# Performance work log

Hardware: AMD Instinct MI355X
Metric: run time of the kernel (lower is better)

## Reference

```python
import jax, jax.numpy as jnp
import numpy as np

B, S, D, E, H, SL = 4, 2048, 2048, 16, 1024, 1
NUM_SLOTS = E * SL
TEMP = 1.0
TOP_K = 2
EPS = 1e-8


def setup_inputs() -> dict:
    key = jax.random.key(0)
    k0, k1, k2, k3 = jax.random.split(key, 4)
    x = jax.random.normal(k0, (B, S, D), dtype=jnp.float32)
    Wd = jax.random.normal(k1, (NUM_SLOTS, D), dtype=jnp.float32) * 0.02
    W1 = jax.random.normal(k2, (E, D, H), dtype=jnp.float32) * 0.02
    b1 = jnp.zeros((E, H), dtype=jnp.float32)
    W2 = jax.random.normal(k3, (E, H, D), dtype=jnp.float32) * 0.02
    b2 = jnp.zeros((E, D), dtype=jnp.float32)
    return {"x": x, "Wd": Wd, "W1": W1, "b1": b1, "W2": W2, "b2": b2}


def reference(x, Wd, W1, b1, W2, b2):
    lead = x.shape[:-1]
    xf = x.reshape(-1, D)                      # [T, D]
    T = xf.shape[0]

    logits = (xf @ Wd.T) / TEMP                # [T, num_slots]
    dispatch = jax.nn.softmax(logits, axis=0)  # softmax over tokens
    combine = jax.nn.softmax(logits, axis=-1)  # softmax over slots

    # Aggregate tokens into slots, run all experts as one batched GEMM chain.
    slot_in = (dispatch.T @ xf).reshape(E, SL, D)                    # [E, SL, D]
    h = jax.nn.gelu(jnp.einsum('esd,edh->esh', slot_in, W1) + b1[:, None, :],
                    approximate=False)
    slot_out = (jnp.einsum('esh,ehd->esd', h, W2) + b2[:, None, :]).reshape(NUM_SLOTS, D)

    out = (combine @ slot_out).reshape(x.shape)

    # Router stats / losses (eval mode: no EMA update of train_scores).
    expert_weights = combine.reshape(T, E, SL).mean(-1)              # [T, E]
    mean_usage = expert_weights.mean(0)                              # [E]
    p = jax.nn.softmax(Wd.mean(0).reshape(E, -1).mean(-1))
    router_loss = E * jnp.sum(mean_usage * p)

    topk_w, topk_idx = jax.lax.top_k(expert_weights, TOP_K)
    topk_w_norm = topk_w / jnp.clip(topk_w.sum(-1, keepdims=True), EPS)

    gate_weights = expert_weights.reshape(*lead, E)
    routing_entropy = -(gate_weights * jnp.log(gate_weights + EPS)).sum(-1).mean()

    return (out,
            router_loss,
            gate_weights,
            topk_idx.reshape(*lead, TOP_K),
            topk_w_norm.reshape(*lead, TOP_K),
            mean_usage,
            routing_entropy,
            dispatch.reshape(*lead, NUM_SLOTS))
```

## Files before the change

kernel.cpp:

```cpp
#include <hip/hip_runtime.h>
#include <math.h>

#define TTOK 8192
#define DIM  2048
#define NH   1024

#define OFF_PART6 0u
#define OFF_NUM   8388608u
#define OFF_COMB  8519680u
#define OFF_CSUM  8650752u
#define OFF_MUSUM 8654848u
#define OFF_ENT   8658944u
#define OFF_SRAW  8659200u
#define OFF_HBUF  8691968u
#define OFF_SLOT  8708352u

#define O_OUT   0u
#define O_LOSS  16777216u
#define O_GATE  16777217u
#define O_TOPI  16908289u
#define O_TOPW  16924673u
#define O_MU    16941057u
#define O_ENTR  16941073u
#define O_DISP  16941074u

__global__ __launch_bounds__(512) void kad(const float* __restrict__ x,
    const float* __restrict__ Wd,
    float* __restrict__ num, float* __restrict__ comb, float* __restrict__ gate_out,
    float* __restrict__ topi_out, float* __restrict__ topw_out,
    float* __restrict__ csum_p, float* __restrict__ musum_p, float* __restrict__ ent_p,
    float* __restrict__ part6){
  const int blk = blockIdx.x;
  const int tid = threadIdx.x;
  const int t0  = blk*32;
  __shared__ float sS[32][17];
  __shared__ __align__(16) float sN[32][16];
  __shared__ float sC[32][16];
  __shared__ float sE[32];

  {
    const int ttp = tid>>5;
    const int kc  = tid&31;
    const float4* xr0 = (const float4*)(x + (size_t)(t0+2*ttp  )*DIM + kc*64);
    const float4* xr1 = (const float4*)(x + (size_t)(t0+2*ttp+1)*DIM + kc*64);
    float a0[16], a1[16];
    #pragma unroll
    for (int e=0;e<16;e++){ a0[e]=0.f; a1[e]=0.f; }
    #pragma unroll
    for (int k4=0;k4<16;k4++){
      float4 x0 = xr0[k4];
      float4 x1 = xr1[k4];
      #pragma unroll
      for (int e=0;e<16;e++){
        float4 w = *(const float4*)(Wd + e*DIM + kc*64 + k4*4);
        a0[e] += x0.x*w.x + x0.y*w.y + x0.z*w.z + x0.w*w.w;
        a1[e] += x1.x*w.x + x1.y*w.y + x1.z*w.z + x1.w*w.w;
      }
    }
    #pragma unroll
    for (int o=1;o<32;o<<=1){
      #pragma unroll
      for (int e=0;e<16;e++){
        a0[e] += __shfl_xor(a0[e],o,64);
        a1[e] += __shfl_xor(a1[e],o,64);
      }
    }
    if (kc==0){
      #pragma unroll
      for (int e=0;e<16;e++){
        sS[2*ttp  ][e] = a0[e];  sN[2*ttp  ][e] = expf(a0[e]);
        sS[2*ttp+1][e] = a1[e];  sN[2*ttp+1][e] = expf(a1[e]);
      }
    }
  }
  __syncthreads();
  if (tid<128) ((float4*)num)[(size_t)blk*128 + tid] = ((const float4*)sN)[tid];
  if (tid<32){
    const int gt = t0 + tid;
    float l[16];
    #pragma unroll
    for (int e=0;e<16;e++) l[e] = sS[tid][e];
    float m = l[0];
    #pragma unroll
    for (int e=1;e<16;e++) m = fmaxf(m,l[e]);
    float c[16]; float sm=0.f;
    #pragma unroll
    for (int e=0;e<16;e++){ c[e]=expf(l[e]-m); sm+=c[e]; }
    float inv = 1.f/sm;
    #pragma unroll
    for (int e=0;e<16;e++) c[e]*=inv;
    float4* co = (float4*)(comb + (size_t)gt*16);
    co[0]=make_float4(c[0],c[1],c[2],c[3]);   co[1]=make_float4(c[4],c[5],c[6],c[7]);
    co[2]=make_float4(c[8],c[9],c[10],c[11]); co[3]=make_float4(c[12],c[13],c[14],c[15]);
    float* go = gate_out + (size_t)gt*16;
    #pragma unroll
    for (int e=0;e<16;e++) go[e]=c[e];
    float v0=-1.f,v1=-1.f; int i0=0,i1=0;
    #pragma unroll
    for (int e=0;e<16;e++){
      float ce=c[e];
      if (ce>v0){ v1=v0;i1=i0; v0=ce;i0=e; }
      else if (ce>v1){ v1=ce;i1=e; }
    }
    float dn = fmaxf(v0+v1,1e-8f);
    topi_out[(size_t)gt*2+0]=(float)i0; topi_out[(size_t)gt*2+1]=(float)i1;
    topw_out[(size_t)gt*2+0]=v0/dn;     topw_out[(size_t)gt*2+1]=v1/dn;
    float ent=0.f;
    #pragma unroll
    for (int e=0;e<16;e++) ent -= c[e]*logf(c[e]+1e-8f);
    sE[tid]=ent;
    #pragma unroll
    for (int e=0;e<16;e++) sC[tid][e]=c[e];
  }
  __syncthreads();
  if (tid<16){
    float ms=0.f, cs=0.f;
    #pragma unroll
    for (int tt=0;tt<32;tt++){ ms += sC[tt][tid]; cs += sN[tt][tid]; }
    musum_p[blk*16+tid]=ms; csum_p[blk*16+tid]=cs;
  }
  if (tid==16){
    float s=0.f;
    #pragma unroll
    for (int k=0;k<32;k++) s += sE[k];
    ent_p[blk]=s;
  }
  __syncthreads();
  {
    float4 acc[16];
    #pragma unroll
    for (int e=0;e<16;e++) acc[e]=make_float4(0,0,0,0);
    #pragma unroll 2
    for (int t=0;t<32;t++){
      const float4 xv = *(const float4*)(x + (size_t)(t0+t)*DIM + tid*4);
      #pragma unroll
      for (int qq=0;qq<4;qq++){
        float4 nq = *((const float4*)&sN[t][qq*4]);
        acc[qq*4+0].x=fmaf(nq.x,xv.x,acc[qq*4+0].x); acc[qq*4+0].y=fmaf(nq.x,xv.y,acc[qq*4+0].y);
        acc[qq*4+0].z=fmaf(nq.x,xv.z,acc[qq*4+0].z); acc[qq*4+0].w=fmaf(nq.x,xv.w,acc[qq*4+0].w);
        acc[qq*4+1].x=fmaf(nq.y,xv.x,acc[qq*4+1].x); acc[qq*4+1].y=fmaf(nq.y,xv.y,acc[qq*4+1].y);
        acc[qq*4+1].z=fmaf(nq.y,xv.z,acc[qq*4+1].z); acc[qq*4+1].w=fmaf(nq.y,xv.w,acc[qq*4+1].w);
        acc[qq*4+2].x=fmaf(nq.z,xv.x,acc[qq*4+2].x); acc[qq*4+2].y=fmaf(nq.z,xv.y,acc[qq*4+2].y);
        acc[qq*4+2].z=fmaf(nq.z,xv.z,acc[qq*4+2].z); acc[qq*4+2].w=fmaf(nq.z,xv.w,acc[qq*4+2].w);
        acc[qq*4+3].x=fmaf(nq.w,xv.x,acc[qq*4+3].x); acc[qq*4+3].y=fmaf(nq.w,xv.y,acc[qq*4+3].y);
        acc[qq*4+3].z=fmaf(nq.w,xv.z,acc[qq*4+3].z); acc[qq*4+3].w=fmaf(nq.w,xv.w,acc[qq*4+3].w);
      }
    }
    #pragma unroll
    for (int e=0;e<16;e++)
      *(float4*)(part6 + ((size_t)blk*16+e)*DIM + tid*4) = acc[e];
  }
}

__global__ __launch_bounds__(256) void ke2(const float* __restrict__ part6,
    const float* __restrict__ csum_p, const float* __restrict__ num,
    const float* __restrict__ musum_p, const float* __restrict__ ent_p,
    const float* __restrict__ Wd,
    float* __restrict__ sraw, float* __restrict__ disp_out,
    float* __restrict__ loss_out, float* __restrict__ mu_out, float* __restrict__ ent_out){
  const int tid = threadIdx.x, blk = blockIdx.x;
  __shared__ float sIv[16][16];
  __shared__ float sInv[16];
  __shared__ float s2[256];
  { int g=tid>>4, e=tid&15;
    float v=0.f;
    #pragma unroll
    for (int k=0;k<16;k++) v += csum_p[(g*16+k)*16 + e];
    sIv[g][e]=v; }
  __syncthreads();
  if (tid<16){
    float v=0.f;
    #pragma unroll
    for (int g=0;g<16;g++) v += sIv[g][tid];
    sInv[tid]=1.f/v;
  }
  __syncthreads();
  { const int ol=tid&31, sl=tid>>5;
    const int o = blk*32 + ol;
    float s=0.f;
    #pragma unroll 8
    for (int k=0;k<32;k++) s += part6[(size_t)(sl*32+k)*32768 + o];
    s2[tid]=s;
  }
  __syncthreads();
  if (tid<32){
    float t=0.f;
    #pragma unroll
    for (int k=0;k<8;k++) t += s2[k*32+tid];
    const int oo = blk*32 + tid;
    sraw[oo] = t * sInv[oo>>11];
  }
  if (blk<512){
    const int t0 = blk*16;
    float v = num[(size_t)t0*16 + tid];
    disp_out[(size_t)t0*16 + tid] = v * sInv[tid&15];
  }
  if (blk==1023){
    __shared__ float sq[16][16];
    __shared__ float smu[16];
    __shared__ float sqv[16];
    __shared__ float sqe[16];
    { int s=tid>>4, ch=tid&15;
      const float* base = Wd + (size_t)s*DIM + ch*128;
      float qv=0.f;
      for (int ii=0;ii<128;ii+=4){ float4 v=*(const float4*)(base+ii); qv+=v.x+v.y+v.z+v.w; }
      sq[s][ch]=qv; }
    if (tid<16){
      float mu=0.f;
      for (int b=0;b<256;b++) mu += musum_p[b*16+tid];
      mu/=8192.f;
      mu_out[tid]=mu; smu[tid]=mu;
    }
    if (tid==32){ float es=0.f; for(int b=0;b<256;b++) es+=ent_p[b]; ent_out[0]=es/8192.f; }
    __syncthreads();
    if (tid<16){ float qv=0.f; for(int s=0;s<16;s++) qv+=sq[s][tid]; sqv[tid]=qv/2048.f; }
    __syncthreads();
    if (tid<16){
      float qm=-INFINITY;
      for (int e=0;e<16;e++) qm=fmaxf(qm,sqv[e]);
      sqe[tid]=expf(sqv[tid]-qm);
    }
    __syncthreads();
    if (tid==0){
      float qs=0.f; for(int e=0;e<16;e++) qs+=sqe[e];
      float loss=0.f; for(int e=0;e<16;e++) loss+=smu[e]*(sqe[e]/qs);
      loss_out[0]=16.f*loss;
    }
  }
}

__global__ __launch_bounds__(256) void kf_h(const float* __restrict__ sraw,
    const float* __restrict__ W1, const float* __restrict__ b1,
    float* __restrict__ hbuf){
  const int e  = blockIdx.x >> 5;
  const int hc = blockIdx.x & 31;
  const int hbase = hc*32;
  const int tid = threadIdx.x;
  __shared__ float sr[2048];
  __shared__ float sacc[256];
  { const float4* s4 = (const float4*)(sraw + (size_t)e*DIM);
    float4 a = s4[tid*2], b = s4[tid*2+1];
    *(float4*)(&sr[tid*8]) = a; *(float4*)(&sr[tid*8+4]) = b; }
  __syncthreads();
  const int hl = tid&31, ds = tid>>5;
  float acc = 0.f;
  const float* wp = W1 + (size_t)e*DIM*NH + hbase + hl;
  #pragma unroll 16
  for (int d2=0; d2<256; d2++){
    const int dd = d2*8 + ds;
    acc = fmaf(sr[dd], wp[(size_t)dd*NH], acc);
  }
  sacc[tid] = acc;
  __syncthreads();
  if (tid < 32){
    float s = 0.f;
    #pragma unroll
    for (int k=0;k<8;k++) s += sacc[k*32 + tid];
    float pre = s + b1[(size_t)e*NH + hbase + tid];
    hbuf[(size_t)e*NH + hbase + tid] = 0.5f*pre*(1.f+erff(pre*0.70710678118654752f));
  }
}

__global__ __launch_bounds__(256) void kg_so(const float* __restrict__ hbuf,
    const float* __restrict__ W2, const float* __restrict__ b2,
    float* __restrict__ slot_out){
  const int e  = blockIdx.x >> 5;
  const int dc = blockIdx.x & 31;
  const int dbase = dc*64;
  const int tid = threadIdx.x;
  __shared__ float hh[1024];
  __shared__ float sacc[256];
  { const float4* h4 = (const float4*)(hbuf + (size_t)e*NH);
    *(float4*)(&hh[tid*4]) = h4[tid]; }
  __syncthreads();
  const int dl = tid&63, hs = tid>>6;
  float acc = 0.f;
  const float* wp = W2 + (size_t)e*NH*DIM + dbase + dl;
  #pragma unroll 16
  for (int h2=0; h2<256; h2++){
    const int hidx = h2*4 + hs;
    acc = fmaf(hh[hidx], wp[(size_t)hidx*DIM], acc);
  }
  sacc[tid] = acc;
  __syncthreads();
  if (tid < 64){
    float s = sacc[tid] + sacc[64+tid] + sacc[128+tid] + sacc[192+tid];
    slot_out[(size_t)e*DIM + dbase + tid] = s + b2[(size_t)e*DIM + dbase + tid];
  }
}

__global__ __launch_bounds__(256) void kh_out(const float* __restrict__ slot_out,
    const float* __restrict__ combine, float* __restrict__ out){
  const int tb = blockIdx.x >> 1;
  const int dc = blockIdx.x & 1;
  const int t0 = tb*16;
  const int d  = dc*1024 + threadIdx.x*4;
  float4 sv[16];
  #pragma unroll
  for (int e=0;e<16;e++) sv[e] = *(const float4*)(slot_out + (size_t)e*DIM + d);
  #pragma unroll 2
  for (int t=0;t<16;t++){
    const float* cr = combine + (size_t)(t0+t)*16;
    float4 a = make_float4(0,0,0,0);
    #pragma unroll
    for (int e=0;e<16;e++){
      float c = cr[e];
      a.x=fmaf(c,sv[e].x,a.x); a.y=fmaf(c,sv[e].y,a.y);
      a.z=fmaf(c,sv[e].z,a.z); a.w=fmaf(c,sv[e].w,a.w);
    }
    *(float4*)(out + (size_t)(t0+t)*DIM + d) = a;
  }
}

extern "C" void kernel_launch(void* const* d_in, const int* in_sizes, int n_in,
                              void* d_out, int out_size, void* d_ws, size_t ws_size,
                              hipStream_t stream) {
  const float* x  = (const float*)d_in[0];
  const float* Wd = (const float*)d_in[1];
  const float* W1 = (const float*)d_in[2];
  const float* b1 = (const float*)d_in[3];
  const float* W2 = (const float*)d_in[4];
  const float* b2 = (const float*)d_in[5];
  float* out = (float*)d_out;
  float* ws  = (float*)d_ws;

  float* part6 = ws + OFF_PART6;
  float* num   = ws + OFF_NUM;
  float* comb  = ws + OFF_COMB;
  float* csump = ws + OFF_CSUM;
  float* musump= ws + OFF_MUSUM;
  float* entp  = ws + OFF_ENT;
  float* sraw  = ws + OFF_SRAW;
  float* hbuf  = ws + OFF_HBUF;
  float* slot  = ws + OFF_SLOT;

  kad<<<256, 512, 0, stream>>>(x, Wd, num, comb, out + O_GATE, out + O_TOPI,
                               out + O_TOPW, csump, musump, entp, part6);
  ke2<<<1024, 256, 0, stream>>>(part6, csump, num, musump, entp, Wd,
                                sraw, out + O_DISP, out + O_LOSS,
                                out + O_MU, out + O_ENTR);
  kf_h<<<512, 256, 0, stream>>>(sraw, W1, b1, hbuf);
  kg_so<<<512, 256, 0, stream>>>(hbuf, W2, b2, slot);
  kh_out<<<1024, 256, 0, stream>>>(slot, comb, out + O_OUT);
}
```

Before: 213.9 us.

## Split fused router kernel into logits, router, and slot-input kernels

Replaces the single 256-block fused kernel with three kernels. The logits kernel runs 1024 blocks that write split-K partial sums to workspace, a router kernel reduces them and computes the softmaxes, top-k and stats, and a slot-input kernel accumulates exp-weighted x across 512 blocks. The goal is more parallelism and occupancy than the fused version with its low block count. The cost is extra kernel launches, a second full read of x, and an 8192x64x16 partial-logit buffer that shares workspace with part6.

New measurement: 204.5 us. -4.4%, faster.

```diff
diff --git a/kernel.cpp b/kernel.cpp
--- a/kernel.cpp
+++ b/kernel.cpp
@@ -5,15 +5,15 @@
 #define DIM  2048
 #define NH   1024
 
-#define OFF_PART6 0u
+#define OFF_ALIAS 0u
 #define OFF_NUM   8388608u
 #define OFF_COMB  8519680u
 #define OFF_CSUM  8650752u
-#define OFF_MUSUM 8654848u
-#define OFF_ENT   8658944u
-#define OFF_SRAW  8659200u
-#define OFF_HBUF  8691968u
-#define OFF_SLOT  8708352u
+#define OFF_MUSUM 8652800u
+#define OFF_ENT   8654848u
+#define OFF_SRAW  8654976u
+#define OFF_HBUF  8687744u
+#define OFF_SLOT  8704128u
 
 #define O_OUT   0u
 #define O_LOSS  16777216u
@@ -24,62 +24,83 @@
 #define O_ENTR  16941073u
 #define O_DISP  16941074u
 
-__global__ __launch_bounds__(512) void kad(const float* __restrict__ x,
-    const float* __restrict__ Wd,
-    float* __restrict__ num, float* __restrict__ comb, float* __restrict__ gate_out,
+__device__ __forceinline__ float wave_sum(float v){
+  #pragma unroll
+  for (int o=1;o<64;o<<=1) v += __shfl_xor(v,o,64);
+  return v;
+}
+
+__global__ __launch_bounds__(256,4) void ka_logits(const float* __restrict__ x,
+                                                   const float* __restrict__ Wd,
+                                                   float* __restrict__ part1){
+  const int tb = blockIdx.x >> 6;
+  const int kc = blockIdx.x & 63;
+  const int t0 = tb*512 + threadIdx.x;
+  const int t1 = t0 + 256;
+  const float4* __restrict__ xr0 = (const float4*)(x + (size_t)t0*DIM + kc*32);
+  const float4* __restrict__ xr1 = (const float4*)(x + (size_t)t1*DIM + kc*32);
+  float a0[16], a1[16];
+  #pragma unroll
+  for (int e=0;e<16;e++){ a0[e]=0.f; a1[e]=0.f; }
+  #pragma unroll
+  for (int k4=0;k4<8;k4++){
+    float4 x0 = xr0[k4];
+    float4 x1 = xr1[k4];
+    #pragma unroll
+    for (int e=0;e<16;e++){
+      float4 w = *(const float4*)(Wd + e*DIM + kc*32 + k4*4);
+      a0[e] += x0.x*w.x + x0.y*w.y + x0.z*w.z + x0.w*w.w;
+      a1[e] += x1.x*w.x + x1.y*w.y + x1.z*w.z + x1.w*w.w;
+    }
+  }
+  float4* p0 = (float4*)(part1 + ((size_t)t0*64 + kc)*16);
+  p0[0]=make_float4(a0[0],a0[1],a0[2],a0[3]);   p0[1]=make_float4(a0[4],a0[5],a0[6],a0[7]);
+  p0[2]=make_float4(a0[8],a0[9],a0[10],a0[11]); p0[3]=make_float4(a0[12],a0[13],a0[14],a0[15]);
+  float4* p1 = (float4*)(part1 + ((size_t)t1*64 + kc)*16);
+  p1[0]=make_float4(a1[0],a1[1],a1[2],a1[3]);   p1[1]=make_float4(a1[4],a1[5],a1[6],a1[7]);
+  p1[2]=make_float4(a1[8],a1[9],a1[10],a1[11]); p1[3]=make_float4(a1[12],a1[13],a1[14],a1[15]);
+}
+
+__global__ __launch_bounds__(256) void kb_router(const float* __restrict__ part1,
+    float* __restrict__ num, float* __restrict__ csum_part,
+    float* __restrict__ combine, float* __restrict__ gate_out,
     float* __restrict__ topi_out, float* __restrict__ topw_out,
-    float* __restrict__ csum_p, float* __restrict__ musum_p, float* __restrict__ ent_p,
-    float* __restrict__ part6){
-  const int blk = blockIdx.x;
+    float* __restrict__ musum_part, float* __restrict__ ent_part){
   const int tid = threadIdx.x;
-  const int t0  = blk*32;
-  __shared__ float sS[32][17];
-  __shared__ __align__(16) float sN[32][16];
-  __shared__ float sC[32][16];
-  __shared__ float sE[32];
-
-  {
-    const int ttp = tid>>5;
-    const int kc  = tid&31;
-    const float4* xr0 = (const float4*)(x + (size_t)(t0+2*ttp  )*DIM + kc*64);
-    const float4* xr1 = (const float4*)(x + (size_t)(t0+2*ttp+1)*DIM + kc*64);
-    float a0[16], a1[16];
-    #pragma unroll
-    for (int e=0;e<16;e++){ a0[e]=0.f; a1[e]=0.f; }
-    #pragma unroll
-    for (int k4=0;k4<16;k4++){
-      float4 x0 = xr0[k4];
-      float4 x1 = xr1[k4];
-      #pragma unroll
-      for (int e=0;e<16;e++){
-        float4 w = *(const float4*)(Wd + e*DIM + kc*64 + k4*4);
-        a0[e] += x0.x*w.x + x0.y*w.y + x0.z*w.z + x0.w*w.w;
-        a1[e] += x1.x*w.x + x1.y*w.y + x1.z*w.z + x1.w*w.w;
-      }
-    }
-    #pragma unroll
-    for (int o=1;o<32;o<<=1){
-      #pragma unroll
-      for (int e=0;e<16;e++){
-        a0[e] += __shfl_xor(a0[e],o,64);
-        a1[e] += __shfl_xor(a1[e],o,64);
-      }
-    }
-    if (kc==0){
-      #pragma unroll
-      for (int e=0;e<16;e++){
-        sS[2*ttp  ][e] = a0[e];  sN[2*ttp  ][e] = expf(a0[e]);
-        sS[2*ttp+1][e] = a1[e];  sN[2*ttp+1][e] = expf(a1[e]);
-      }
-    }
-  }
-  __syncthreads();
-  if (tid<128) ((float4*)num)[(size_t)blk*128 + tid] = ((const float4*)sN)[tid];
-  if (tid<32){
-    const int gt = t0 + tid;
+  const int i = blockIdx.x*256 + tid;
+  const float4* p1 = (const float4*)part1;
+  const size_t base = (size_t)(i>>2)*256 + (i&3);
+  float4 s = make_float4(0,0,0,0);
+  #pragma unroll 8
+  for (int kc=0;kc<64;kc++){
+    float4 v = p1[base + kc*4];
+    s.x+=v.x; s.y+=v.y; s.z+=v.z; s.w+=v.w;
+  }
+  float4 n4 = make_float4(expf(s.x),expf(s.y),expf(s.z),expf(s.w));
+  ((float4*)num)[i] = n4;
+  __shared__ float Lg[64][20];
+  const int tl = tid>>2, q = tid&3;
+  *(float4*)(&Lg[tl][q*4]) = s;
+  float4 n = n4;
+  #pragma unroll
+  for (int o=4;o<64;o<<=1){
+    n.x += __shfl_xor(n.x,o,64); n.y += __shfl_xor(n.y,o,64);
+    n.z += __shfl_xor(n.z,o,64); n.w += __shfl_xor(n.w,o,64);
+  }
+  __shared__ float4 red[4][4];
+  const int w = tid>>6, lane = tid&63;
+  if (lane<4) red[w][lane] = n;
+  __syncthreads();
+  if (tid<4){
+    float4 a=red[0][tid],b=red[1][tid],c=red[2][tid],d=red[3][tid];
+    *(float4*)(csum_part + blockIdx.x*16 + tid*4) =
+      make_float4(a.x+b.x+c.x+d.x, a.y+b.y+c.y+d.y, a.z+b.z+c.z+d.z, a.w+b.w+c.w+d.w);
+  }
+  if (tid < 64){
+    const int gt = blockIdx.x*64 + tid;
     float l[16];
     #pragma unroll
-    for (int e=0;e<16;e++) l[e] = sS[tid][e];
+    for (int e=0;e<16;e++) l[e] = Lg[tid][e];
     float m = l[0];
     #pragma unroll
     for (int e=1;e<16;e++) m = fmaxf(m,l[e]);
@@ -89,67 +110,67 @@
     float inv = 1.f/sm;
     #pragma unroll
     for (int e=0;e<16;e++) c[e]*=inv;
-    float4* co = (float4*)(comb + (size_t)gt*16);
+    float4* co = (float4*)(combine + (size_t)gt*16);
     co[0]=make_float4(c[0],c[1],c[2],c[3]);   co[1]=make_float4(c[4],c[5],c[6],c[7]);
     co[2]=make_float4(c[8],c[9],c[10],c[11]); co[3]=make_float4(c[12],c[13],c[14],c[15]);
     float* go = gate_out + (size_t)gt*16;
     #pragma unroll
     for (int e=0;e<16;e++) go[e]=c[e];
-    float v0=-1.f,v1=-1.f; int i0=0,i1=0;
+    float v0=-1.f, v1=-1.f; int i0=0, i1=0;
     #pragma unroll
     for (int e=0;e<16;e++){
       float ce=c[e];
-      if (ce>v0){ v1=v0;i1=i0; v0=ce;i0=e; }
-      else if (ce>v1){ v1=ce;i1=e; }
-    }
-    float dn = fmaxf(v0+v1,1e-8f);
+      if (ce>v0){ v1=v0; i1=i0; v0=ce; i0=e; }
+      else if (ce>v1){ v1=ce; i1=e; }
+    }
+    float dn = fmaxf(v0+v1, 1e-8f);
     topi_out[(size_t)gt*2+0]=(float)i0; topi_out[(size_t)gt*2+1]=(float)i1;
     topw_out[(size_t)gt*2+0]=v0/dn;     topw_out[(size_t)gt*2+1]=v1/dn;
     float ent=0.f;
     #pragma unroll
     for (int e=0;e<16;e++) ent -= c[e]*logf(c[e]+1e-8f);
-    sE[tid]=ent;
-    #pragma unroll
-    for (int e=0;e<16;e++) sC[tid][e]=c[e];
-  }
-  __syncthreads();
-  if (tid<16){
-    float ms=0.f, cs=0.f;
-    #pragma unroll
-    for (int tt=0;tt<32;tt++){ ms += sC[tt][tid]; cs += sN[tt][tid]; }
-    musum_p[blk*16+tid]=ms; csum_p[blk*16+tid]=cs;
-  }
-  if (tid==16){
-    float s=0.f;
-    #pragma unroll
-    for (int k=0;k<32;k++) s += sE[k];
-    ent_p[blk]=s;
-  }
-  __syncthreads();
-  {
-    float4 acc[16];
-    #pragma unroll
-    for (int e=0;e<16;e++) acc[e]=make_float4(0,0,0,0);
-    #pragma unroll 2
-    for (int t=0;t<32;t++){
-      const float4 xv = *(const float4*)(x + (size_t)(t0+t)*DIM + tid*4);
-      #pragma unroll
-      for (int qq=0;qq<4;qq++){
-        float4 nq = *((const float4*)&sN[t][qq*4]);
-        acc[qq*4+0].x=fmaf(nq.x,xv.x,acc[qq*4+0].x); acc[qq*4+0].y=fmaf(nq.x,xv.y,acc[qq*4+0].y);
-        acc[qq*4+0].z=fmaf(nq.x,xv.z,acc[qq*4+0].z); acc[qq*4+0].w=fmaf(nq.x,xv.w,acc[qq*4+0].w);
-        acc[qq*4+1].x=fmaf(nq.y,xv.x,acc[qq*4+1].x); acc[qq*4+1].y=fmaf(nq.y,xv.y,acc[qq*4+1].y);
-        acc[qq*4+1].z=fmaf(nq.y,xv.z,acc[qq*4+1].z); acc[qq*4+1].w=fmaf(nq.y,xv.w,acc[qq*4+1].w);
-        acc[qq*4+2].x=fmaf(nq.z,xv.x,acc[qq*4+2].x); acc[qq*4+2].y=fmaf(nq.z,xv.y,acc[qq*4+2].y);
-        acc[qq*4+2].z=fmaf(nq.z,xv.z,acc[qq*4+2].z); acc[qq*4+2].w=fmaf(nq.z,xv.w,acc[qq*4+2].w);
-        acc[qq*4+3].x=fmaf(nq.w,xv.x,acc[qq*4+3].x); acc[qq*4+3].y=fmaf(nq.w,xv.y,acc[qq*4+3].y);
-        acc[qq*4+3].z=fmaf(nq.w,xv.z,acc[qq*4+3].z); acc[qq*4+3].w=fmaf(nq.w,xv.w,acc[qq*4+3].w);
-      }
-    }
-    #pragma unroll
-    for (int e=0;e<16;e++)
-      *(float4*)(part6 + ((size_t)blk*16+e)*DIM + tid*4) = acc[e];
-  }
+    #pragma unroll
+    for (int e=0;e<16;e++){
+      float v = wave_sum(c[e]);
+      if (tid==0) musum_part[blockIdx.x*16+e] = v;
+    }
+    float ve = wave_sum(ent);
+    if (tid==0) ent_part[blockIdx.x] = ve;
+  }
+}
+
+__global__ __launch_bounds__(256) void kd_slotin(const float* __restrict__ x,
+    const float* __restrict__ num, float* __restrict__ part6){
+  const int tc = blockIdx.x >> 1;
+  const int dc = blockIdx.x & 1;
+  const int tid = threadIdx.x;
+  const int d  = dc*1024 + tid*4;
+  const int t0 = tc*32;
+  __shared__ float4 sN[128];
+  if (tid < 128) sN[tid] = ((const float4*)num)[t0*4 + tid];
+  __syncthreads();
+  float4 acc[16];
+  #pragma unroll
+  for (int e=0;e<16;e++) acc[e]=make_float4(0,0,0,0);
+  #pragma unroll 2
+  for (int t=0;t<32;t++){
+    const float4 xv = *(const float4*)(x + (size_t)(t0+t)*DIM + d);
+    #pragma unroll
+    for (int qq=0;qq<4;qq++){
+      float4 nq = sN[t*4+qq];
+      acc[qq*4+0].x=fmaf(nq.x,xv.x,acc[qq*4+0].x); acc[qq*4+0].y=fmaf(nq.x,xv.y,acc[qq*4+0].y);
+      acc[qq*4+0].z=fmaf(nq.x,xv.z,acc[qq*4+0].z); acc[qq*4+0].w=fmaf(nq.x,xv.w,acc[qq*4+0].w);
+      acc[qq*4+1].x=fmaf(nq.y,xv.x,acc[qq*4+1].x); acc[qq*4+1].y=fmaf(nq.y,xv.y,acc[qq*4+1].y);
+      acc[qq*4+1].z=fmaf(nq.y,xv.z,acc[qq*4+1].z); acc[qq*4+1].w=fmaf(nq.y,xv.w,acc[qq*4+1].w);
+      acc[qq*4+2].x=fmaf(nq.z,xv.x,acc[qq*4+2].x); acc[qq*4+2].y=fmaf(nq.z,xv.y,acc[qq*4+2].y);
+      acc[qq*4+2].z=fmaf(nq.z,xv.z,acc[qq*4+2].z); acc[qq*4+2].w=fmaf(nq.z,xv.w,acc[qq*4+2].w);
+      acc[qq*4+3].x=fmaf(nq.w,xv.x,acc[qq*4+3].x); acc[qq*4+3].y=fmaf(nq.w,xv.y,acc[qq*4+3].y);
+      acc[qq*4+3].z=fmaf(nq.w,xv.z,acc[qq*4+3].z); acc[qq*4+3].w=fmaf(nq.w,xv.w,acc[qq*4+3].w);
+    }
+  }
+  #pragma unroll
+  for (int e=0;e<16;e++)
+    *(float4*)(part6 + ((size_t)tc*16+e)*DIM + d) = acc[e];
 }
 
 __global__ __launch_bounds__(256) void ke2(const float* __restrict__ part6,
@@ -165,7 +186,7 @@
   { int g=tid>>4, e=tid&15;
     float v=0.f;
     #pragma unroll
-    for (int k=0;k<16;k++) v += csum_p[(g*16+k)*16 + e];
+    for (int k=0;k<8;k++) v += csum_p[(g*8+k)*16 + e];
     sIv[g][e]=v; }
   __syncthreads();
   if (tid<16){
@@ -207,11 +228,11 @@
       sq[s][ch]=qv; }
     if (tid<16){
       float mu=0.f;
-      for (int b=0;b<256;b++) mu += musum_p[b*16+tid];
+      for (int b=0;b<128;b++) mu += musum_p[b*16+tid];
       mu/=8192.f;
       mu_out[tid]=mu; smu[tid]=mu;
     }
-    if (tid==32){ float es=0.f; for(int b=0;b<256;b++) es+=ent_p[b]; ent_out[0]=es/8192.f; }
+    if (tid==32){ float es=0.f; for(int b=0;b<128;b++) es+=ent_p[b]; ent_out[0]=es/8192.f; }
     __syncthreads();
     if (tid<16){ float qv=0.f; for(int s=0;s<16;s++) qv+=sq[s][tid]; sqv[tid]=qv/2048.f; }
     __syncthreads();
@@ -324,7 +345,8 @@
   float* out = (float*)d_out;
   float* ws  = (float*)d_ws;
 
-  float* part6 = ws + OFF_PART6;
+  float* part1 = ws + OFF_ALIAS;
+  float* part6 = ws + OFF_ALIAS;
   float* num   = ws + OFF_NUM;
   float* comb  = ws + OFF_COMB;
   float* csump = ws + OFF_CSUM;
@@ -334,8 +356,10 @@
   float* hbuf  = ws + OFF_HBUF;
   float* slot  = ws + OFF_SLOT;
 
-  kad<<<256, 512, 0, stream>>>(x, Wd, num, comb, out + O_GATE, out + O_TOPI,
-                               out + O_TOPW, csump, musump, entp, part6);
+  ka_logits<<<1024, 256, 0, stream>>>(x, Wd, part1);
+  kb_router<<<128, 256, 0, stream>>>(part1, num, csump, comb, out + O_GATE,
+                                     out + O_TOPI, out + O_TOPW, musump, entp);
+  kd_slotin<<<512, 256, 0, stream>>>(x, num, part6);
   ke2<<<1024, 256, 0, stream>>>(part6, csump, num, musump, entp, Wd,
                                 sraw, out + O_DISP, out + O_LOSS,
                                 out + O_MU, out + O_ENTR);
```
